# Kernel tuning notes

Measured on AMD Instinct MI355X. Metric: run time of the kernel, lower is better.

The kernel has to match this reference:

```python
import jax, jax.numpy as jnp
import numpy as np

N_NODES = 100000   # num_nodes_ori
N_EDGES = 1600000  # avg degree 16
D_IN = 128
D_OUT = 128


def setup_inputs() -> dict:
    key = jax.random.key(0)
    k_x, k_w, k_r, k_c, k_v = jax.random.split(key, 5)
    stdv = 1.0 / np.sqrt(D_OUT).astype(np.float32)
    X = jax.random.normal(k_x, (N_NODES, D_IN), dtype=jnp.float32)
    weights = jax.random.uniform(k_w, (D_IN, D_OUT), jnp.float32, -stdv, stdv)
    # CSR-equivalent edge list of the normalized adjacency A (values = norm coeffs)
    edge_rows = jnp.sort(jax.random.randint(k_r, (N_EDGES,), 0, N_NODES, dtype=jnp.int32))
    edge_cols = jax.random.randint(k_c, (N_EDGES,), 0, N_NODES, dtype=jnp.int32)
    edge_vals = jax.random.uniform(k_v, (N_EDGES,), jnp.float32)
    return {"X": X, "weights": weights, "edge_rows": edge_rows,
            "edge_cols": edge_cols, "edge_vals": edge_vals}


def reference(X, weights, edge_rows, edge_cols, edge_vals):
    # Dense feature transform: X' = X @ W   [N, D_OUT]
    XW = jnp.matmul(X, weights)
    # Sparse aggregation out = A @ X' (edge-list SpMM, same math as Libra6SpMM):
    # gather source features, scale by edge value, scatter-add into dst rows.
    msgs = XW[edge_cols] * edge_vals[:, None]            # [E, D_OUT]
    out = jax.ops.segment_sum(msgs, edge_rows, num_segments=N_NODES)
    return out
```

## Files before the change

kernel.cpp:

```cpp
#include <hip/hip_runtime.h>

#define D 128

typedef __attribute__((ext_vector_type(8))) short bf16x8;
typedef __attribute__((ext_vector_type(4))) float f32x4;
typedef __attribute__((ext_vector_type(2))) float f32x2;
typedef __attribute__((ext_vector_type(2))) uint  u32x2;

__device__ __forceinline__ ushort f2bf(float f) {
    unsigned u = __float_as_uint(f);
    u += 0x7fffu + ((u >> 16) & 1u);
    return (ushort)(u >> 16);
}
__device__ __forceinline__ float bf2f(ushort h) {
    return __uint_as_float(((unsigned)h) << 16);
}

__global__ __launch_bounds__(256) void gemm_mfma(const float* __restrict__ X,
                                                 const float* __restrict__ W,
                                                 const int* __restrict__ rows,
                                                 int E,
                                                 ushort* __restrict__ XW,
                                                 int* __restrict__ rp, int M) {
    __shared__ ushort Wl[16384];

    const int t = threadIdx.x;

    {
        const int g = blockIdx.x * 256 + t;
        if (g <= M) {
            int lo = 0, hi = E;
            while (lo < hi) {
                int mid = (lo + hi) >> 1;
                if (rows[mid] < g) lo = mid + 1; else hi = mid;
            }
            rp[g] = lo;
        }
    }

    {
        const int c = t & 127, half = t >> 7;
        const int jt = c >> 4;
#pragma unroll
        for (int g = 0; g < 8; ++g) {
            const int k8   = half + g * 2;
            const int ks   = k8 >> 2;
            const int lsub = (k8 & 3) * 16 + (c & 15);
            uint4 pk;
            ushort tmp[8];
#pragma unroll
            for (int j = 0; j < 8; ++j)
                tmp[j] = f2bf(W[(k8 * 8 + j) * D + c]);
            pk.x = (uint)tmp[0] | ((uint)tmp[1] << 16);
            pk.y = (uint)tmp[2] | ((uint)tmp[3] << 16);
            pk.z = (uint)tmp[4] | ((uint)tmp[5] << 16);
            pk.w = (uint)tmp[6] | ((uint)tmp[7] << 16);
            *(uint4*)&Wl[(((jt * 4 + ks) * 64) + lsub) * 8] = pk;
        }
    }

    const int lane = t & 63, wid = t >> 6;
    const int r0 = blockIdx.x * 64 + wid * 16;

    int arow = r0 + (lane & 15);
    if (arow >= M) arow = M - 1;
    const float* xp = X + (size_t)arow * D + ((lane >> 4) * 8);

    bf16x8 xf[4];
#pragma unroll
    for (int ks = 0; ks < 4; ++ks) {
        float4 f0 = *(const float4*)(xp + ks * 32);
        float4 f1 = *(const float4*)(xp + ks * 32 + 4);
        bf16x8 av;
        av[0] = (short)f2bf(f0.x); av[1] = (short)f2bf(f0.y);
        av[2] = (short)f2bf(f0.z); av[3] = (short)f2bf(f0.w);
        av[4] = (short)f2bf(f1.x); av[5] = (short)f2bf(f1.y);
        av[6] = (short)f2bf(f1.z); av[7] = (short)f2bf(f1.w);
        xf[ks] = av;
    }

    __syncthreads();

    const bf16x8* wl = (const bf16x8*)Wl + lane;

    f32x4 acc[8];
#pragma unroll
    for (int jt = 0; jt < 8; ++jt) acc[jt] = (f32x4){0.f, 0.f, 0.f, 0.f};

#pragma unroll
    for (int jt = 0; jt < 8; ++jt)
#pragma unroll
        for (int ks = 0; ks < 4; ++ks) {
            bf16x8 w = wl[(jt * 4 + ks) * 64];
            acc[jt] = __builtin_amdgcn_mfma_f32_16x16x32_bf16(w, xf[ks],
                                                              acc[jt], 0, 0, 0);
        }

    const int row = r0 + (lane & 15);
    if (row < M) {
        uint* dst = (uint*)XW + (size_t)row * 64 + (lane >> 4) * 2;
#pragma unroll
        for (int jt = 0; jt < 8; ++jt) {
            u32x2 pv;
            pv[0] = (uint)f2bf(acc[jt][0]) | ((uint)f2bf(acc[jt][1]) << 16);
            pv[1] = (uint)f2bf(acc[jt][2]) | ((uint)f2bf(acc[jt][3]) << 16);
            *(u32x2*)(dst + jt * 8) = pv;
        }
    }
}

__global__ __launch_bounds__(256) void spmm_csr(const ushort* __restrict__ XW,
                                                const int* __restrict__ rp,
                                                const int* __restrict__ cols,
                                                const float* __restrict__ vals,
                                                float* __restrict__ out, int N) {
    const int lane = threadIdx.x & 63;
    const int ra = blockIdx.x * 8 + (threadIdx.x >> 6) * 2;
    if (ra >= N) return;
    const bool has_b = (ra + 1) < N;

    const int sa = rp[ra];
    const int ea = rp[ra + 1];
    const int eb = has_b ? rp[ra + 2] : ea;

    const uint* base = (const uint*)XW;
    float axa = 0.f, aya = 0.f, axb = 0.f, ayb = 0.f;

    int ia = sa, ib = ea;

    while (ia + 4 <= ea && ib + 4 <= eb) {
        int c0[4], c1[4]; float v0[4], v1[4]; uint u0[4], u1[4];
#pragma unroll
        for (int q = 0; q < 4; ++q) {
            c0[q] = __builtin_nontemporal_load(&cols[ia + q]);
            c1[q] = __builtin_nontemporal_load(&cols[ib + q]);
            v0[q] = __builtin_nontemporal_load(&vals[ia + q]);
            v1[q] = __builtin_nontemporal_load(&vals[ib + q]);
        }
#pragma unroll
        for (int q = 0; q < 4; ++q) {
            u0[q] = base[(size_t)c0[q] * 64 + lane];
            u1[q] = base[(size_t)c1[q] * 64 + lane];
        }
#pragma unroll
        for (int q = 0; q < 4; ++q) {
            axa += v0[q] * bf2f((ushort)(u0[q] & 0xffff));
            aya += v0[q] * bf2f((ushort)(u0[q] >> 16));
            axb += v1[q] * bf2f((ushort)(u1[q] & 0xffff));
            ayb += v1[q] * bf2f((ushort)(u1[q] >> 16));
        }
        ia += 4; ib += 4;
    }
    for (; ia + 4 <= ea; ia += 4) {
        int c[4]; float v[4]; uint u[4];
#pragma unroll
        for (int q = 0; q < 4; ++q) {
            c[q] = __builtin_nontemporal_load(&cols[ia + q]);
            v[q] = __builtin_nontemporal_load(&vals[ia + q]);
        }
#pragma unroll
        for (int q = 0; q < 4; ++q) u[q] = base[(size_t)c[q] * 64 + lane];
#pragma unroll
        for (int q = 0; q < 4; ++q) {
            axa += v[q] * bf2f((ushort)(u[q] & 0xffff));
            aya += v[q] * bf2f((ushort)(u[q] >> 16));
        }
    }
    for (; ia < ea; ++ia) {
        int c = cols[ia]; float v = vals[ia];
        uint u = base[(size_t)c * 64 + lane];
        axa += v * bf2f((ushort)(u & 0xffff));
        aya += v * bf2f((ushort)(u >> 16));
    }
    for (; ib + 4 <= eb; ib += 4) {
        int c[4]; float v[4]; uint u[4];
#pragma unroll
        for (int q = 0; q < 4; ++q) {
            c[q] = __builtin_nontemporal_load(&cols[ib + q]);
            v[q] = __builtin_nontemporal_load(&vals[ib + q]);
        }
#pragma unroll
        for (int q = 0; q < 4; ++q) u[q] = base[(size_t)c[q] * 64 + lane];
#pragma unroll
        for (int q = 0; q < 4; ++q) {
            axb += v[q] * bf2f((ushort)(u[q] & 0xffff));
            ayb += v[q] * bf2f((ushort)(u[q] >> 16));
        }
    }
    for (; ib < eb; ++ib) {
        int c = cols[ib]; float v = vals[ib];
        uint u = base[(size_t)c * 64 + lane];
        axb += v * bf2f((ushort)(u & 0xffff));
        ayb += v * bf2f((ushort)(u >> 16));
    }

    f32x2 oa; oa[0] = axa; oa[1] = aya;
    __builtin_nontemporal_store(oa, (f32x2*)out + (size_t)ra * 64 + lane);
    if (has_b) {
        f32x2 ob; ob[0] = axb; ob[1] = ayb;
        __builtin_nontemporal_store(ob, (f32x2*)out + (size_t)(ra + 1) * 64 + lane);
    }
}

extern "C" void kernel_launch(void* const* d_in, const int* in_sizes, int n_in,
                              void* d_out, int out_size, void* d_ws, size_t ws_size,
                              hipStream_t stream) {
    const float* X    = (const float*)d_in[0];
    const float* W    = (const float*)d_in[1];
    const int*   rows = (const int*)d_in[2];
    const int*   cols = (const int*)d_in[3];
    const float* vals = (const float*)d_in[4];
    float*       out  = (float*)d_out;

    const int M = in_sizes[0] / D;
    const int E = in_sizes[2];

    ushort* XWb = (ushort*)d_ws;
    int*    rp  = (int*)((char*)d_ws + (size_t)M * D * sizeof(ushort));

    gemm_mfma<<<(M + 63) / 64, 256, 0, stream>>>(X, W, rows, E, XWb, rp, M);
    spmm_csr <<<(M + 7) / 8, 256, 0, stream>>>(XWb, rp, cols, vals, out, M);
}
```

Measured before the change: 198.3 us.

## Partition edges by source-column range and aggregate in synchronized phases

Adds a reorg kernel that buckets each row's edges into four column-range phases and packs col/val into one 64-bit word. A new SpMM kernel handles 6 rows per wave and walks the phases in order with block syncs between them, so concurrently running waves gather from a narrower slice of XW. The aim is better L2/cache locality for the random gathers and fewer separate index loads. The cost is an extra kernel pass over all edges, writes of the reordered array, and phase barriers that may serialize work unevenly.

```diff
diff --git a/kernel.cpp b/kernel.cpp
--- a/kernel.cpp
+++ b/kernel.cpp
@@ -109,6 +109,112 @@
     }
 }
 
+__global__ __launch_bounds__(256) void reorg_edges(const int* __restrict__ rp,
+                                                   const int* __restrict__ cols,
+                                                   const float* __restrict__ vals,
+                                                   long long* __restrict__ colv,
+                                                   int4* __restrict__ off,
+                                                   int N, float inv_psize) {
+    const int lane = threadIdx.x & 63;
+    const int r = blockIdx.x * 4 + (threadIdx.x >> 6);
+    if (r >= N) return;
+    const int s = rp[r], e = rp[r + 1];
+
+    int cnt0 = 0, cnt1 = 0, cnt2 = 0;
+    for (int base = s; base < e; base += 64) {
+        const bool act = (base + lane) < e;
+        int c = act ? cols[base + lane] : 0;
+        int ph = (int)((float)c * inv_psize); ph = ph > 3 ? 3 : ph;
+        cnt0 += __popcll(__ballot(act && ph == 0));
+        cnt1 += __popcll(__ballot(act && ph == 1));
+        cnt2 += __popcll(__ballot(act && ph == 2));
+    }
+    const int st0 = s, st1 = st0 + cnt0, st2 = st1 + cnt1, st3 = st2 + cnt2;
+    if (lane == 0) off[r] = make_int4(st0, st1, st2, st3);
+
+    int d0 = 0, d1 = 0, d2 = 0, d3 = 0;
+    for (int base = s; base < e; base += 64) {
+        const bool act = (base + lane) < e;
+        int   c = act ? cols[base + lane] : 0;
+        float v = act ? vals[base + lane] : 0.f;
+        int ph = (int)((float)c * inv_psize); ph = ph > 3 ? 3 : ph;
+        unsigned long long b0 = __ballot(act && ph == 0);
+        unsigned long long b1 = __ballot(act && ph == 1);
+        unsigned long long b2 = __ballot(act && ph == 2);
+        unsigned long long b3 = __ballot(act && ph == 3);
+        unsigned long long lmlt = (1ull << lane) - 1ull;
+        unsigned long long bm = ph == 0 ? b0 : ph == 1 ? b1 : ph == 2 ? b2 : b3;
+        int stp = ph == 0 ? st0 : ph == 1 ? st1 : ph == 2 ? st2 : st3;
+        int dnp = ph == 0 ? d0  : ph == 1 ? d1  : ph == 2 ? d2  : d3;
+        if (act) {
+            int pos = stp + dnp + __popcll(bm & lmlt);
+            colv[pos] = (long long)(unsigned)c |
+                        ((long long)(unsigned)__float_as_uint(v) << 32);
+        }
+        d0 += __popcll(b0); d1 += __popcll(b1);
+        d2 += __popcll(b2); d3 += __popcll(b3);
+    }
+}
+
+#define RW 6
+#define BR 24
+__global__ __launch_bounds__(256, 4) void spmm_phased(
+        const ushort* __restrict__ XW, const int* __restrict__ rp,
+        const int4* __restrict__ off, const long long* __restrict__ colv,
+        float* __restrict__ out, int N) {
+    const int lane = threadIdx.x & 63;
+    const int wid  = threadIdx.x >> 6;
+    const int r0 = blockIdx.x * BR + wid * RW;
+    const uint* base = (const uint*)XW;
+
+    float ax[RW], ay[RW];
+#pragma unroll
+    for (int k = 0; k < RW; ++k) { ax[k] = 0.f; ay[k] = 0.f; }
+
+#pragma unroll
+    for (int p = 0; p < 4; ++p) {
+#pragma unroll
+        for (int k = 0; k < RW; ++k) {
+            const int r = r0 + k;
+            if (r >= N) continue;
+            const int4 o = off[r];
+            const int s = p == 0 ? o.x : p == 1 ? o.y : p == 2 ? o.z : o.w;
+            const int e = p == 3 ? rp[r + 1] : (p == 0 ? o.y : p == 1 ? o.z : o.w);
+            float axk = ax[k], ayk = ay[k];
+            for (int i = s; i < e; i += 4) {
+                long long cv[4];
+#pragma unroll
+                for (int q = 0; q < 4; ++q) {
+                    int idx = i + q; idx = idx < e ? idx : e - 1;
+                    cv[q] = __builtin_nontemporal_load(&colv[idx]);
+                }
+                uint u[4];
+#pragma unroll
+                for (int q = 0; q < 4; ++q)
+                    u[q] = base[(size_t)(uint)(cv[q] & 0xffffffffll) * 64 + lane];
+#pragma unroll
+                for (int q = 0; q < 4; ++q) {
+                    float v = (i + q < e)
+                              ? __uint_as_float((uint)(cv[q] >> 32)) : 0.f;
+                    axk += v * bf2f((ushort)(u[q] & 0xffff));
+                    ayk += v * bf2f((ushort)(u[q] >> 16));
+                }
+            }
+            ax[k] = axk; ay[k] = ayk;
+        }
+        __syncthreads();
+    }
+
+#pragma unroll
+    for (int k = 0; k < RW; ++k) {
+        const int r = r0 + k;
+        if (r < N) {
+            f32x2 o2; o2[0] = ax[k]; o2[1] = ay[k];
+            __builtin_nontemporal_store(o2, (f32x2*)out + (size_t)r * 64 + lane);
+        }
+    }
+}
+
 __global__ __launch_bounds__(256) void spmm_csr(const ushort* __restrict__ XW,
                                                 const int* __restrict__ rp,
                                                 const int* __restrict__ cols,
@@ -125,7 +231,6 @@
 
     const uint* base = (const uint*)XW;
     float axa = 0.f, aya = 0.f, axb = 0.f, ayb = 0.f;
-
     int ia = sa, ib = ea;
 
     while (ia + 4 <= ea && ib + 4 <= eb) {
@@ -151,41 +256,11 @@
         }
         ia += 4; ib += 4;
     }
-    for (; ia + 4 <= ea; ia += 4) {
-        int c[4]; float v[4]; uint u[4];
-#pragma unroll
-        for (int q = 0; q < 4; ++q) {
-            c[q] = __builtin_nontemporal_load(&cols[ia + q]);
-            v[q] = __builtin_nontemporal_load(&vals[ia + q]);
-        }
-#pragma unroll
-        for (int q = 0; q < 4; ++q) u[q] = base[(size_t)c[q] * 64 + lane];
-#pragma unroll
-        for (int q = 0; q < 4; ++q) {
-            axa += v[q] * bf2f((ushort)(u[q] & 0xffff));
-            aya += v[q] * bf2f((ushort)(u[q] >> 16));
-        }
-    }
     for (; ia < ea; ++ia) {
         int c = cols[ia]; float v = vals[ia];
         uint u = base[(size_t)c * 64 + lane];
         axa += v * bf2f((ushort)(u & 0xffff));
         aya += v * bf2f((ushort)(u >> 16));
-    }
-    for (; ib + 4 <= eb; ib += 4) {
-        int c[4]; float v[4]; uint u[4];
-#pragma unroll
-        for (int q = 0; q < 4; ++q) {
-            c[q] = __builtin_nontemporal_load(&cols[ib + q]);
-            v[q] = __builtin_nontemporal_load(&vals[ib + q]);
-        }
-#pragma unroll
-        for (int q = 0; q < 4; ++q) u[q] = base[(size_t)c[q] * 64 + lane];
-#pragma unroll
-        for (int q = 0; q < 4; ++q) {
-            axb += v[q] * bf2f((ushort)(u[q] & 0xffff));
-            ayb += v[q] * bf2f((ushort)(u[q] >> 16));
-        }
     }
     for (; ib < eb; ++ib) {
         int c = cols[ib]; float v = vals[ib];
@@ -215,9 +290,27 @@
     const int M = in_sizes[0] / D;
     const int E = in_sizes[2];
 
-    ushort* XWb = (ushort*)d_ws;
-    int*    rp  = (int*)((char*)d_ws + (size_t)M * D * sizeof(ushort));
+    char* ws = (char*)d_ws;
+    size_t o_xw   = 0;
+    size_t o_rp   = o_xw + (size_t)M * D * sizeof(ushort);
+    size_t o_off  = (o_rp + (size_t)(M + 1) * sizeof(int) + 15) & ~(size_t)15;
+    size_t o_colv = o_off + (size_t)M * sizeof(int4);
+    size_t need   = o_colv + (size_t)E * sizeof(long long);
+
+    ushort*    XWb  = (ushort*)(ws + o_xw);
+    int*       rp   = (int*)(ws + o_rp);
+    int4*      off  = (int4*)(ws + o_off);
+    long long* colv = (long long*)(ws + o_colv);
 
     gemm_mfma<<<(M + 63) / 64, 256, 0, stream>>>(X, W, rows, E, XWb, rp, M);
-    spmm_csr <<<(M + 7) / 8, 256, 0, stream>>>(XWb, rp, cols, vals, out, M);
-}
+
+    if (ws_size >= need) {
+        const float inv_psize = 1.0f / (float)((M + 3) / 4);
+        reorg_edges<<<(M + 3) / 4, 256, 0, stream>>>(rp, cols, vals, colv, off,
+                                                     M, inv_psize);
+        spmm_phased<<<(M + BR - 1) / BR, 256, 0, stream>>>(XWb, rp, off, colv,
+                                                           out, M);
+    } else {
+        spmm_csr<<<(M + 7) / 8, 256, 0, stream>>>(XWb, rp, cols, vals, out, M);
+    }
+}
```

After: 300.8 us. 1.52x slower.

## Split GEMM into prep (bf16 convert, W pre-layout, rowptr) and lean MFMA kernel

Applied to the files above, without the earlier changes.

Adds a prep kernel that converts X to bf16, lays W out in MFMA fragment order in global memory, and builds the CSR row pointers. A lean GEMM kernel then reads the bf16 X and fragment-ordered W directly, with no per-block W conversion into LDS and no __syncthreads. This removes the W conversion that every block repeated, but adds an extra launch and a full write and read of a bf16 copy of X. The SpMM single-row 4-way unrolled tails are also removed in favour of scalar loops.

```diff
diff --git a/kernel.cpp b/kernel.cpp
--- a/kernel.cpp
+++ b/kernel.cpp
@@ -16,16 +16,101 @@
     return __uint_as_float(((unsigned)h) << 16);
 }
 
-__global__ __launch_bounds__(256) void gemm_mfma(const float* __restrict__ X,
-                                                 const float* __restrict__ W,
-                                                 const int* __restrict__ rows,
-                                                 int E,
-                                                 ushort* __restrict__ XW,
-                                                 int* __restrict__ rp, int M) {
+__global__ __launch_bounds__(256) void prep(const float* __restrict__ X,
+                                            const float* __restrict__ W,
+                                            const int* __restrict__ rows,
+                                            ushort* __restrict__ Xb,
+                                            ushort* __restrict__ Wf,
+                                            int* __restrict__ rp,
+                                            int M, int E, int nXchunks) {
+    const int b = blockIdx.x, t = threadIdx.x;
+
+    const int idx8 = b * 256 + t;
+    if (idx8 < nXchunks) {
+        const float4 f0 = *(const float4*)(X + (size_t)idx8 * 8);
+        const float4 f1 = *(const float4*)(X + (size_t)idx8 * 8 + 4);
+        bf16x8 o;
+        o[0] = (short)f2bf(f0.x); o[1] = (short)f2bf(f0.y);
+        o[2] = (short)f2bf(f0.z); o[3] = (short)f2bf(f0.w);
+        o[4] = (short)f2bf(f1.x); o[5] = (short)f2bf(f1.y);
+        o[6] = (short)f2bf(f1.z); o[7] = (short)f2bf(f1.w);
+        *(bf16x8*)(Xb + (size_t)idx8 * 8) = o;
+    }
+
+    if (b < 64) {
+        const int idx = b * 256 + t;
+        const int j    = idx & 7;
+        const int lane = (idx >> 3) & 63;
+        const int f    = idx >> 9;
+        const int jt = f >> 2, ks = f & 3;
+        const int col = jt * 16 + (lane & 15);
+        const int k   = ks * 32 + ((lane >> 4) * 8) + j;
+        Wf[idx] = f2bf(W[k * D + col]);
+    }
+
+    const int g = (b - 64) * 256 + t;
+    if (b >= 64 && g <= M) {
+        int lo = 0, hi = E;
+        while (lo < hi) {
+            int mid = (lo + hi) >> 1;
+            if (rows[mid] < g) lo = mid + 1; else hi = mid;
+        }
+        rp[g] = lo;
+    }
+}
+
+__global__ __launch_bounds__(256) void gemm_lean(const ushort* __restrict__ Xb,
+                                                 const ushort* __restrict__ Wf,
+                                                 ushort* __restrict__ XW, int M) {
+    const int t = threadIdx.x, lane = t & 63, wid = t >> 6;
+    const int r0 = blockIdx.x * 64 + wid * 16;
+
+    int arow = r0 + (lane & 15);
+    if (arow >= M) arow = M - 1;
+    const ushort* xp = Xb + (size_t)arow * D + ((lane >> 4) * 8);
+
+    bf16x8 xf[4];
+#pragma unroll
+    for (int ks = 0; ks < 4; ++ks)
+        xf[ks] = *(const bf16x8*)(xp + ks * 32);
+
+    const bf16x8* wf = (const bf16x8*)Wf + lane;
+
+    f32x4 acc[8];
+#pragma unroll
+    for (int jt = 0; jt < 8; ++jt) acc[jt] = (f32x4){0.f, 0.f, 0.f, 0.f};
+
+#pragma unroll
+    for (int jt = 0; jt < 8; ++jt)
+#pragma unroll
+        for (int ks = 0; ks < 4; ++ks) {
+            bf16x8 w = wf[(jt * 4 + ks) * 64];
+            acc[jt] = __builtin_amdgcn_mfma_f32_16x16x32_bf16(w, xf[ks],
+                                                              acc[jt], 0, 0, 0);
+        }
+
+    const int row = r0 + (lane & 15);
+    if (row < M) {
+        uint* dst = (uint*)XW + (size_t)row * 64 + (lane >> 4) * 2;
+#pragma unroll
+        for (int jt = 0; jt < 8; ++jt) {
+            u32x2 pv;
+            pv[0] = (uint)f2bf(acc[jt][0]) | ((uint)f2bf(acc[jt][1]) << 16);
+            pv[1] = (uint)f2bf(acc[jt][2]) | ((uint)f2bf(acc[jt][3]) << 16);
+            *(u32x2*)(dst + jt * 8) = pv;
+        }
+    }
+}
+
+__global__ __launch_bounds__(256) void gemm_fused(const float* __restrict__ X,
+                                                  const float* __restrict__ W,
+                                                  const int* __restrict__ rows,
+                                                  int E,
+                                                  ushort* __restrict__ XW,
+                                                  int* __restrict__ rp, int M) {
     __shared__ ushort Wl[16384];
 
     const int t = threadIdx.x;
-
     {
         const int g = blockIdx.x * 256 + t;
         if (g <= M) {
@@ -37,7 +122,6 @@
             rp[g] = lo;
         }
     }
-
     {
         const int c = t & 127, half = t >> 7;
         const int jt = c >> 4;
@@ -125,7 +209,6 @@
 
     const uint* base = (const uint*)XW;
     float axa = 0.f, aya = 0.f, axb = 0.f, ayb = 0.f;
-
     int ia = sa, ib = ea;
 
     while (ia + 4 <= ea && ib + 4 <= eb) {
@@ -151,41 +234,11 @@
         }
         ia += 4; ib += 4;
     }
-    for (; ia + 4 <= ea; ia += 4) {
-        int c[4]; float v[4]; uint u[4];
-#pragma unroll
-        for (int q = 0; q < 4; ++q) {
-            c[q] = __builtin_nontemporal_load(&cols[ia + q]);
-            v[q] = __builtin_nontemporal_load(&vals[ia + q]);
-        }
-#pragma unroll
-        for (int q = 0; q < 4; ++q) u[q] = base[(size_t)c[q] * 64 + lane];
-#pragma unroll
-        for (int q = 0; q < 4; ++q) {
-            axa += v[q] * bf2f((ushort)(u[q] & 0xffff));
-            aya += v[q] * bf2f((ushort)(u[q] >> 16));
-        }
-    }
     for (; ia < ea; ++ia) {
         int c = cols[ia]; float v = vals[ia];
         uint u = base[(size_t)c * 64 + lane];
         axa += v * bf2f((ushort)(u & 0xffff));
         aya += v * bf2f((ushort)(u >> 16));
-    }
-    for (; ib + 4 <= eb; ib += 4) {
-        int c[4]; float v[4]; uint u[4];
-#pragma unroll
-        for (int q = 0; q < 4; ++q) {
-            c[q] = __builtin_nontemporal_load(&cols[ib + q]);
-            v[q] = __builtin_nontemporal_load(&vals[ib + q]);
-        }
-#pragma unroll
-        for (int q = 0; q < 4; ++q) u[q] = base[(size_t)c[q] * 64 + lane];
-#pragma unroll
-        for (int q = 0; q < 4; ++q) {
-            axb += v[q] * bf2f((ushort)(u[q] & 0xffff));
-            ayb += v[q] * bf2f((ushort)(u[q] >> 16));
-        }
     }
     for (; ib < eb; ++ib) {
         int c = cols[ib]; float v = vals[ib];
@@ -215,9 +268,27 @@
     const int M = in_sizes[0] / D;
     const int E = in_sizes[2];
 
-    ushort* XWb = (ushort*)d_ws;
-    int*    rp  = (int*)((char*)d_ws + (size_t)M * D * sizeof(ushort));
-
-    gemm_mfma<<<(M + 63) / 64, 256, 0, stream>>>(X, W, rows, E, XWb, rp, M);
-    spmm_csr <<<(M + 7) / 8, 256, 0, stream>>>(XWb, rp, cols, vals, out, M);
-}
+    char* ws = (char*)d_ws;
+    size_t o_xw = 0;
+    size_t o_rp = o_xw + (size_t)M * D * sizeof(ushort);
+    size_t o_wf = (o_rp + (size_t)(M + 1) * sizeof(int) + 15) & ~(size_t)15;
+    size_t o_xb = o_wf + (size_t)16384 * sizeof(ushort);
+    size_t need = o_xb + (size_t)M * D * sizeof(ushort);
+
+    ushort* XWb = (ushort*)(ws + o_xw);
+    int*    rp  = (int*)(ws + o_rp);
+    ushort* Wf  = (ushort*)(ws + o_wf);
+    ushort* Xb  = (ushort*)(ws + o_xb);
+
+    if (ws_size >= need) {
+        const int nXchunks = M * (D / 8);
+        const int rowptr_blocks = (M + 256) / 256;
+        int grid = (nXchunks + 255) / 256;
+        if (grid < 64 + rowptr_blocks) grid = 64 + rowptr_blocks;
+        prep<<<grid, 256, 0, stream>>>(X, W, rows, Xb, Wf, rp, M, E, nXchunks);
+        gemm_lean<<<(M + 63) / 64, 256, 0, stream>>>(Xb, Wf, XWb, M);
+    } else {
+        gemm_fused<<<(M + 63) / 64, 256, 0, stream>>>(X, W, rows, E, XWb, rp, M);
+    }
+    spmm_csr<<<(M + 7) / 8, 256, 0, stream>>>(XWb, rp, cols, vals, out, M);
+}
```

New measurement: 229.6 us. 15.8% more time.
